# Kernel tuning notes

Measured on AMD Instinct MI355X. Metric: run time of the kernel, lower is better.

The kernel has to match this reference:

```python
import jax, jax.numpy as jnp
import numpy as np

NUM_CLASSES = 37
NUM_INSTANCE = 2
FEAT_LEN = 256
N = 262144


def setup_inputs() -> dict:
    key = jax.random.key(0)
    k1, k2 = jax.random.split(key)
    features = jax.random.normal(k1, (N, FEAT_LEN), dtype=jnp.float32)
    pid_labels = jax.random.randint(k2, (N,), 0, NUM_CLASSES, dtype=jnp.int64)
    large_batch_queue = jnp.zeros((NUM_CLASSES, NUM_INSTANCE, FEAT_LEN), dtype=jnp.float32)
    tail = jnp.zeros((NUM_CLASSES,), dtype=jnp.int64)
    return {
        "features": features,
        "pid_labels": pid_labels,
        "large_batch_queue": large_batch_queue,
        "tail": tail,
    }


def reference(features, pid_labels, large_batch_queue, tail):
    # Fused segment-mean + scatter into rotating queue.
    C, I, F = large_batch_queue.shape  # [37, 2, 256]
    # Per-class sums and counts in one pass over features (replaces per-class loop).
    sums = jax.ops.segment_sum(features, pid_labels, num_segments=C)          # [C, F]
    counts = jax.ops.segment_sum(
        jnp.ones((features.shape[0],), dtype=features.dtype), pid_labels, num_segments=C
    )                                                                          # [C]
    present = counts > 0
    mean = sums / jnp.maximum(counts, 1.0)[:, None]                            # [C, F]
    rows = jnp.arange(C)
    cur = large_batch_queue[rows, tail]                                        # [C, F] current slot
    new_vals = jnp.where(present[:, None], mean, cur)
    new_queue = large_batch_queue.at[rows, tail].set(new_vals)
    # tail rotates modulo queue depth for present classes (mirrors +=1 then wrap);
    # original returns only the queue buffer.
    return new_queue
```

## Files before the change

kernel.cpp:

```cpp
#include <hip/hip_runtime.h>


constexpr int C   = 37;
constexpr int F   = 256;
constexpr int WPB = 4;

__global__ __launch_bounds__(256) void k_accum(
    const float* __restrict__ feat, const int* __restrict__ labels,
    float* __restrict__ psums, float* __restrict__ pcnts, int rpw)
{
    __shared__ float ls[WPB][C * F];
    __shared__ int   lcnt[WPB][64];
    const int t = threadIdx.x;
    const int w = t >> 6;
    const int l = t & 63;

    float4* lz = (float4*)ls[w];
    for (int i = l; i < C * F / 4; i += 64)
        lz[i] = make_float4(0.f, 0.f, 0.f, 0.f);

    const size_t rbase = (size_t)blockIdx.x * (size_t)(rpw * WPB) + (size_t)w * rpw;
    const float4* f4 = (const float4*)feat;

    int cnt = 0;

    float4 buf[8]; int cls[8];
    #pragma unroll
    for (int k = 0; k < 8; ++k) {
        buf[k] = f4[(rbase + k) * 64 + l];
        cls[k] = labels[rbase + k];
    }

    for (int i = 0; i < rpw; i += 8) {
        float4 nbuf[8]; int ncls[8];
        const bool more = (i + 8) < rpw;
        if (more) {
            #pragma unroll
            for (int k = 0; k < 8; ++k) {
                nbuf[k] = f4[(rbase + i + 8 + k) * 64 + l];
                ncls[k] = labels[rbase + i + 8 + k];
            }
        }
        #pragma unroll
        for (int k = 0; k < 8; ++k) {
            const int c = cls[k];
            cnt += (c == l);
            float4* p = (float4*)&ls[w][c * F + 4 * l];
            float4 a = *p;
            a.x += buf[k].x; a.y += buf[k].y; a.z += buf[k].z; a.w += buf[k].w;
            *p = a;
        }
        if (more) {
            #pragma unroll
            for (int k = 0; k < 8; ++k) { buf[k] = nbuf[k]; cls[k] = ncls[k]; }
        }
    }

    lcnt[w][l] = cnt;
    __syncthreads();

    float* po = psums + (size_t)blockIdx.x * (C * F);
    for (int i = t; i < C * F; i += 256)
        po[i] = ls[0][i] + ls[1][i] + ls[2][i] + ls[3][i];
    if (t < C)
        pcnts[(size_t)blockIdx.x * C + t] =
            (float)(lcnt[0][t] + lcnt[1][t] + lcnt[2][t] + lcnt[3][t]);
}

__global__ __launch_bounds__(256) void k_reduce(
    const float* __restrict__ psums, float* __restrict__ s2, int per_stripe)
{
    const int c = blockIdx.x;
    const int s = blockIdx.y;
    const int t = threadIdx.x;
    const int b0 = s * per_stripe;
    float acc = 0.f;
    #pragma unroll 8
    for (int b = b0; b < b0 + per_stripe; ++b)
        acc += psums[((size_t)b * C + c) * F + t];
    s2[((size_t)s * C + c) * F + t] = acc;
}

__global__ __launch_bounds__(256) void k_final(
    const float* __restrict__ s2, const float* __restrict__ pcnts,
    const float* __restrict__ queue, const int* __restrict__ tail,
    float* __restrict__ out, int NB, int S)
{
    const int c = blockIdx.x;
    const int t = threadIdx.x;

    float s = 0.f;
    for (int k = 0; k < S; ++k) s += s2[((size_t)k * C + c) * F + t];

    __shared__ float red[256];
    float cnt = 0.f;
    for (int b = t; b < NB; b += 256) cnt += pcnts[(size_t)b * C + c];
    red[t] = cnt;
    __syncthreads();
    for (int off = 128; off > 0; off >>= 1) {
        if (t < off) red[t] += red[t + off];
        __syncthreads();
    }
    const float total = red[0];

    int tl = tail[c];
    tl = tl < 0 ? 0 : (tl > 1 ? 1 : tl);
    const bool  present = total > 0.f;
    const float mean    = s / fmaxf(total, 1.f);

    const float q0 = queue[((size_t)c * 2 + 0) * F + t];
    const float q1 = queue[((size_t)c * 2 + 1) * F + t];
    float o0 = q0, o1 = q1;
    if (tl == 0) o0 = present ? mean : q0;
    else         o1 = present ? mean : q1;
    out[((size_t)c * 2 + 0) * F + t] = o0;
    out[((size_t)c * 2 + 1) * F + t] = o1;
}

extern "C" void kernel_launch(void* const* d_in, const int* in_sizes, int n_in,
                              void* d_out, int out_size, void* d_ws, size_t ws_size,
                              hipStream_t stream)
{
    const float* feat   = (const float*)d_in[0];
    const int*   labels = (const int*)d_in[1];
    const float* queue  = (const float*)d_in[2];
    const int*   tail   = (const int*)d_in[3];
    float* out = (float*)d_out;
    float* ws  = (float*)d_ws;

    const int N = in_sizes[1];
    const int S = 8;

    int NB = 256;
    while (NB > 32) {
        size_t need = ((size_t)NB * C * F + (size_t)NB * C + (size_t)S * C * F + 64) * sizeof(float);
        if (need <= ws_size) break;
        NB >>= 1;
    }
    const int rpw = N / (NB * WPB);

    float* psums = ws;
    float* pcnts = psums + (size_t)NB * C * F;
    float* s2    = pcnts + (size_t)NB * C;

    hipLaunchKernelGGL(k_accum,  dim3(NB),   dim3(256), 0, stream,
                       feat, labels, psums, pcnts, rpw);
    hipLaunchKernelGGL(k_reduce, dim3(C, S), dim3(256), 0, stream,
                       psums, s2, NB / S);
    hipLaunchKernelGGL(k_final,  dim3(C),    dim3(256), 0, stream,
                       s2, pcnts, queue, tail, out, NB, S);
}
```

Baseline: 56.49 us.

## Fuse partial-sum reduction and final queue update into one tail kernel

Merges the stripe reduction kernel and the final mean/scatter kernel into a single kernel with a (C,4) grid. Each block's four wavefronts sum a quarter of the per-block partials for 64 columns, combine through shared memory, and write the queue output. This removes one kernel launch and the round trip through the intermediate s2 buffer. The cost is fewer blocks (148 instead of 296) for the reduction, each doing longer serial load loops.

```diff
diff --git a/kernel.cpp b/kernel.cpp
--- a/kernel.cpp
+++ b/kernel.cpp
@@ -67,54 +67,70 @@
             (float)(lcnt[0][t] + lcnt[1][t] + lcnt[2][t] + lcnt[3][t]);
 }
 
-__global__ __launch_bounds__(256) void k_reduce(
-    const float* __restrict__ psums, float* __restrict__ s2, int per_stripe)
+__global__ __launch_bounds__(256) void k_tail(
+    const float* __restrict__ psums, const float* __restrict__ pcnts,
+    const float* __restrict__ queue, const int* __restrict__ tail,
+    float* __restrict__ out, int NB)
 {
-    const int c = blockIdx.x;
-    const int s = blockIdx.y;
-    const int t = threadIdx.x;
-    const int b0 = s * per_stripe;
-    float acc = 0.f;
-    #pragma unroll 8
-    for (int b = b0; b < b0 + per_stripe; ++b)
-        acc += psums[((size_t)b * C + c) * F + t];
-    s2[((size_t)s * C + c) * F + t] = acc;
-}
+    const int c  = blockIdx.x;
+    const int q  = blockIdx.y;
+    const int t  = threadIdx.x;
+    const int cl = t & 63;
+    const int bs = t >> 6;
+    const int col = q * 64 + cl;
+    const int npb = NB >> 2;
 
-__global__ __launch_bounds__(256) void k_final(
-    const float* __restrict__ s2, const float* __restrict__ pcnts,
-    const float* __restrict__ queue, const int* __restrict__ tail,
-    float* __restrict__ out, int NB, int S)
-{
-    const int c = blockIdx.x;
-    const int t = threadIdx.x;
+    float a0 = 0.f, a1 = 0.f, a2 = 0.f, a3 = 0.f;
+    float a4 = 0.f, a5 = 0.f, a6 = 0.f, a7 = 0.f;
+    const size_t stride = (size_t)C * F;
+    const float* p = psums + (size_t)(bs * npb) * stride + (size_t)c * F + col;
+    for (int b = 0; b < npb; b += 8) {
+        a0 += p[(size_t)(b + 0) * stride];
+        a1 += p[(size_t)(b + 1) * stride];
+        a2 += p[(size_t)(b + 2) * stride];
+        a3 += p[(size_t)(b + 3) * stride];
+        a4 += p[(size_t)(b + 4) * stride];
+        a5 += p[(size_t)(b + 5) * stride];
+        a6 += p[(size_t)(b + 6) * stride];
+        a7 += p[(size_t)(b + 7) * stride];
+    }
+    const float acc = ((a0 + a1) + (a2 + a3)) + ((a4 + a5) + (a6 + a7));
 
-    float s = 0.f;
-    for (int k = 0; k < S; ++k) s += s2[((size_t)k * C + c) * F + t];
-
-    __shared__ float red[256];
+    __shared__ float reds[256];
+    __shared__ float redc[256];
+    reds[t] = acc;
     float cnt = 0.f;
     for (int b = t; b < NB; b += 256) cnt += pcnts[(size_t)b * C + c];
-    red[t] = cnt;
+    redc[t] = cnt;
     __syncthreads();
-    for (int off = 128; off > 0; off >>= 1) {
-        if (t < off) red[t] += red[t + off];
-        __syncthreads();
+
+    if (t < 64) {
+        const float s = ((reds[t] + reds[t + 64]) + (reds[t + 128] + reds[t + 192]));
+        float total = 0.f;
+        #pragma unroll
+        for (int k = 0; k < 4; ++k) total += redc[t + 64 * k];
+        float tot = redc[0];
+        (void)tot;
+        float ctot = total;
+        #pragma unroll
+        for (int off = 32; off > 0; off >>= 1)
+            ctot += __shfl_down(ctot, off, 64);
+        ctot = __shfl(ctot, 0, 64);
+
+        const bool  present = ctot > 0.f;
+        const float mean    = s / fmaxf(ctot, 1.f);
+
+        int tl = tail[c];
+        tl = tl < 0 ? 0 : (tl > 1 ? 1 : tl);
+
+        const float q0 = queue[((size_t)c * 2 + 0) * F + col];
+        const float q1 = queue[((size_t)c * 2 + 1) * F + col];
+        float o0 = q0, o1 = q1;
+        if (tl == 0) o0 = present ? mean : q0;
+        else         o1 = present ? mean : q1;
+        out[((size_t)c * 2 + 0) * F + col] = o0;
+        out[((size_t)c * 2 + 1) * F + col] = o1;
     }
-    const float total = red[0];
-
-    int tl = tail[c];
-    tl = tl < 0 ? 0 : (tl > 1 ? 1 : tl);
-    const bool  present = total > 0.f;
-    const float mean    = s / fmaxf(total, 1.f);
-
-    const float q0 = queue[((size_t)c * 2 + 0) * F + t];
-    const float q1 = queue[((size_t)c * 2 + 1) * F + t];
-    float o0 = q0, o1 = q1;
-    if (tl == 0) o0 = present ? mean : q0;
-    else         o1 = present ? mean : q1;
-    out[((size_t)c * 2 + 0) * F + t] = o0;
-    out[((size_t)c * 2 + 1) * F + t] = o1;
 }
 
 extern "C" void kernel_launch(void* const* d_in, const int* in_sizes, int n_in,
@@ -129,11 +145,10 @@
     float* ws  = (float*)d_ws;
 
     const int N = in_sizes[1];
-    const int S = 8;
 
     int NB = 256;
     while (NB > 32) {
-        size_t need = ((size_t)NB * C * F + (size_t)NB * C + (size_t)S * C * F + 64) * sizeof(float);
+        size_t need = ((size_t)NB * C * F + (size_t)NB * C + 64) * sizeof(float);
         if (need <= ws_size) break;
         NB >>= 1;
     }
@@ -141,12 +156,9 @@
 
     float* psums = ws;
     float* pcnts = psums + (size_t)NB * C * F;
-    float* s2    = pcnts + (size_t)NB * C;
 
-    hipLaunchKernelGGL(k_accum,  dim3(NB),   dim3(256), 0, stream,
+    hipLaunchKernelGGL(k_accum, dim3(NB),      dim3(256), 0, stream,
                        feat, labels, psums, pcnts, rpw);
-    hipLaunchKernelGGL(k_reduce, dim3(C, S), dim3(256), 0, stream,
-                       psums, s2, NB / S);
-    hipLaunchKernelGGL(k_final,  dim3(C),    dim3(256), 0, stream,
-                       s2, pcnts, queue, tail, out, NB, S);
+    hipLaunchKernelGGL(k_tail,  dim3(C, 4),    dim3(256), 0, stream,
+                       psums, pcnts, queue, tail, out, NB);
 }
```

Measured after the change: 54.69 us. 1.03x faster.
